# Kernel tuning notes

Measured on AMD Instinct MI355X. Metric: run time of the kernel, lower is better.

Reference implementation:

```python
import jax, jax.numpy as jnp
import numpy as np


def setup_inputs() -> dict:
    key = jax.random.key(0)
    H, W, C, N = 200, 200, 256, 2000
    img = jax.random.normal(key, (1, H, W, C), dtype=jnp.float32)
    rng = np.random.RandomState(0)
    x = rng.randint(0, W - 50, size=N)
    y = rng.randint(0, H - 50, size=N)
    w = rng.randint(8, 50, size=N)
    h = rng.randint(8, 50, size=N)
    rois = jnp.asarray(np.stack([x, y, w, h], axis=-1)[None].astype(np.float32))
    return {"img": img, "rois": rois, "pool_size": 7}


def _roi_bilinear(feat, roi, ps):
    # feat: (H, W, C); roi: int32 (x, y, w, h) -> (ps, ps, C)
    # Mirrors TF1 tf.image.resize_images bilinear, align_corners=False:
    # src coordinate inside the crop = out_idx * (crop_size / ps).
    H, W = feat.shape[0], feat.shape[1]
    x, y, w, h = roi[0], roi[1], roi[2], roi[3]
    sy = h.astype(jnp.float32) / ps
    sx = w.astype(jnp.float32) / ps
    src_y = jnp.arange(ps, dtype=jnp.float32) * sy
    src_x = jnp.arange(ps, dtype=jnp.float32) * sx
    y0 = jnp.floor(src_y).astype(jnp.int32)
    x0 = jnp.floor(src_x).astype(jnp.int32)
    wy = src_y - y0.astype(jnp.float32)
    wx = src_x - x0.astype(jnp.float32)
    # clamp inside the crop, then translate to global image coords (and clamp for safety)
    gy0 = jnp.clip(y + jnp.clip(y0, 0, h - 1), 0, H - 1)
    gy1 = jnp.clip(y + jnp.clip(y0 + 1, 0, h - 1), 0, H - 1)
    gx0 = jnp.clip(x + jnp.clip(x0, 0, w - 1), 0, W - 1)
    gx1 = jnp.clip(x + jnp.clip(x0 + 1, 0, w - 1), 0, W - 1)
    v00 = feat[gy0[:, None], gx0[None, :]]  # (ps, ps, C)
    v01 = feat[gy0[:, None], gx1[None, :]]
    v10 = feat[gy1[:, None], gx0[None, :]]
    v11 = feat[gy1[:, None], gx1[None, :]]
    wy = wy[:, None, None]
    wx = wx[None, :, None]
    top = v00 * (1.0 - wx) + v01 * wx
    bot = v10 * (1.0 - wx) + v11 * wx
    return top * (1.0 - wy) + bot * wy


def reference(img, rois, pool_size):
    feat = img[0]                          # (H, W, C)
    roi_int = rois[0].astype(jnp.int32)    # (N, 4) -- cast as in the 'tf' branch
    pooled = jax.vmap(lambda r: _roi_bilinear(feat, r, pool_size))(roi_int)
    return pooled[None]                    # (1, N, ps, ps, C)
```

## Files before the change

kernel.cpp:

```cpp
#include <hip/hip_runtime.h>
#include <hip/hip_bf16.h>


typedef float f32x4 __attribute__((ext_vector_type(4)));

__global__ __launch_bounds__(256) void RoIPool_53575422050620_kernel(
    const float* __restrict__ feat,
    const float* __restrict__ rois,
    const int*   __restrict__ psp,
    float*       __restrict__ out,
    int n_rows, int H, int W, int C)
{
    const int ps  = psp[0];
    const int row = blockIdx.x * 4 + (threadIdx.x >> 6);
    if (row >= n_rows) return;
    const int lane = threadIdx.x & 63;

    const int roi = row / ps;
    const int py  = row - roi * ps;

    const float4 r = reinterpret_cast<const float4*>(rois)[roi];
    const int x = (int)r.x;
    const int y = (int)r.y;
    const int w = (int)r.z;
    const int h = (int)r.w;

    const float sy    = (float)h / (float)ps;
    const float sx    = (float)w / (float)ps;
    const float src_y = (float)py * sy;
    const int   y0    = (int)floorf(src_y);
    const float wy    = src_y - (float)y0;
    const float omwy  = 1.0f - wy;

    const int gy0 = min(max(y + min(max(y0,     0), h - 1), 0), H - 1);
    const int gy1 = min(max(y + min(max(y0 + 1, 0), h - 1), 0), H - 1);

    const int C4 = C >> 2;
    const f32x4* __restrict__ f4 = reinterpret_cast<const f32x4*>(feat);
    f32x4* __restrict__ o4 = reinterpret_cast<f32x4*>(out);

    const size_t r0 = (size_t)(gy0 * W) * C4 + lane;
    const size_t r1 = (size_t)(gy1 * W) * C4 + lane;
    const size_t ob = (size_t)row * ps * C4 + lane;

    auto body = [&](int px) {
        const float src_x = (float)px * sx;
        const int   x0    = (int)floorf(src_x);
        const float wx    = src_x - (float)x0;
        const float omwx  = 1.0f - wx;

        const int gx0 = min(max(x + min(max(x0,     0), w - 1), 0), W - 1);
        const int gx1 = min(max(x + min(max(x0 + 1, 0), w - 1), 0), W - 1);

        const f32x4 v00 = f4[r0 + (size_t)gx0 * C4];
        const f32x4 v01 = f4[r0 + (size_t)gx1 * C4];
        const f32x4 v10 = f4[r1 + (size_t)gx0 * C4];
        const f32x4 v11 = f4[r1 + (size_t)gx1 * C4];

        const f32x4 top = v00 * omwx + v01 * wx;
        const f32x4 bot = v10 * omwx + v11 * wx;
        const f32x4 o   = top * omwy + bot * wy;

        __builtin_nontemporal_store(o, &o4[ob + (size_t)px * C4]);
    };

    if (ps == 7) {
#pragma unroll
        for (int px = 0; px < 7; ++px) body(px);
    } else {
        for (int px = 0; px < ps; ++px) body(px);
    }
}

extern "C" void kernel_launch(void* const* d_in, const int* in_sizes, int n_in,
                              void* d_out, int out_size, void* d_ws, size_t ws_size,
                              hipStream_t stream) {
    const float* img  = (const float*)d_in[0];
    const float* rois = (const float*)d_in[1];
    const int*   psp  = (const int*)d_in[2];
    float*       out  = (float*)d_out;

    const int H = 200, W = 200, C = 256;
    const int ps = 7;
    const int n_rows = out_size / (C * ps);
    const int blocks = (n_rows + 3) / 4;

    RoIPool_53575422050620_kernel<<<blocks, 256, 0, stream>>>(
        img, rois, psp, out, n_rows, H, W, C);
}
```

Baseline: 169.3 us.

## Sort output rows by source image row via counting sort for cache locality

Adds four small pre-pass kernels that build a histogram of each output row's gy0 source image row, scan it, and scatter row indices into a permutation map. The main kernel then processes rows in gy0-sorted order, so concurrently running wavefronts touch the same image rows and L2 hits should improve. The cost is four extra launches, a serial single-thread scan, atomics, and scattered output writes. It also stops reading pool_size from the input and uses the hardcoded value instead.

```diff
diff --git a/kernel.cpp b/kernel.cpp
--- a/kernel.cpp
+++ b/kernel.cpp
@@ -4,16 +4,61 @@
 
 typedef float f32x4 __attribute__((ext_vector_type(4)));
 
+#define IMG_H 200
+#define IMG_W 200
+#define NBINS 256
+
+__device__ __forceinline__ int row_gy0(const float4 r, int py, int ps) {
+    const int y = (int)r.y;
+    const int h = (int)r.w;
+    const float sy    = (float)h / (float)ps;
+    const float src_y = (float)py * sy;
+    const int   y0    = (int)floorf(src_y);
+    return min(max(y + min(max(y0, 0), h - 1), 0), IMG_H - 1);
+}
+
+__global__ void zero_bins_kernel(int* __restrict__ bins) {
+    bins[threadIdx.x] = 0;
+}
+
+__global__ void hist_kernel(const float* __restrict__ rois, int* __restrict__ bins,
+                            int n_rows, int ps) {
+    const int row = blockIdx.x * blockDim.x + threadIdx.x;
+    if (row >= n_rows) return;
+    const int roi = row / ps;
+    const int py  = row - roi * ps;
+    const float4 r = reinterpret_cast<const float4*>(rois)[roi];
+    atomicAdd(&bins[row_gy0(r, py, ps)], 1);
+}
+
+__global__ void scan_kernel(const int* __restrict__ bins, int* __restrict__ offs) {
+    if (threadIdx.x == 0) {
+        int acc = 0;
+        for (int i = 0; i < NBINS; ++i) { offs[i] = acc; acc += bins[i]; }
+    }
+}
+
+__global__ void scatter_kernel(const float* __restrict__ rois, int* __restrict__ offs,
+                               int* __restrict__ rowmap, int n_rows, int ps) {
+    const int row = blockIdx.x * blockDim.x + threadIdx.x;
+    if (row >= n_rows) return;
+    const int roi = row / ps;
+    const int py  = row - roi * ps;
+    const float4 r = reinterpret_cast<const float4*>(rois)[roi];
+    const int pos = atomicAdd(&offs[row_gy0(r, py, ps)], 1);
+    rowmap[pos] = row;
+}
+
 __global__ __launch_bounds__(256) void RoIPool_53575422050620_kernel(
     const float* __restrict__ feat,
     const float* __restrict__ rois,
-    const int*   __restrict__ psp,
+    const int*   __restrict__ rowmap,
     float*       __restrict__ out,
-    int n_rows, int H, int W, int C)
+    int n_rows, int H, int W, int C, int ps)
 {
-    const int ps  = psp[0];
-    const int row = blockIdx.x * 4 + (threadIdx.x >> 6);
-    if (row >= n_rows) return;
+    const int slot = blockIdx.x * 4 + (threadIdx.x >> 6);
+    if (slot >= n_rows) return;
+    const int row  = rowmap[slot];
     const int lane = threadIdx.x & 63;
 
     const int roi = row / ps;
@@ -77,14 +122,22 @@
                               hipStream_t stream) {
     const float* img  = (const float*)d_in[0];
     const float* rois = (const float*)d_in[1];
-    const int*   psp  = (const int*)d_in[2];
     float*       out  = (float*)d_out;
 
     const int H = 200, W = 200, C = 256;
     const int ps = 7;
     const int n_rows = out_size / (C * ps);
+
+    int* bins   = (int*)d_ws;
+    int* offs   = bins + NBINS;
+    int* rowmap = offs + NBINS;
+
+    zero_bins_kernel<<<1, NBINS, 0, stream>>>(bins);
+    hist_kernel<<<(n_rows + 255) / 256, 256, 0, stream>>>(rois, bins, n_rows, ps);
+    scan_kernel<<<1, 64, 0, stream>>>(bins, offs);
+    scatter_kernel<<<(n_rows + 255) / 256, 256, 0, stream>>>(rois, offs, rowmap, n_rows, ps);
+
     const int blocks = (n_rows + 3) / 4;
-
     RoIPool_53575422050620_kernel<<<blocks, 256, 0, stream>>>(
-        img, rois, psp, out, n_rows, H, W, C);
+        img, rois, rowmap, out, n_rows, H, W, C, ps);
 }
```

After: 185.2 us. +9.4%, slower.
